# Optimization experiments

Measured on AMD Instinct MI355X. Metric: run time of the kernel, lower is better.

The kernel has to match this reference:

```python
import jax, jax.numpy as jnp
import numpy as np

B, S, H, E, K = 2, 2048, 1024, 8, 2
CAP_FACTOR = 1.5

def setup_inputs() -> dict:
    key = jax.random.key(0)
    ks = jax.random.split(key, 8)
    sd1 = 1.0 / np.sqrt(H)
    sd2 = 1.0 / np.sqrt(H + E)
    return {
        'hidden_states': jax.random.normal(ks[0], (B, S, H), dtype=jnp.float32),
        'w1': jax.random.normal(ks[1], (H, H), dtype=jnp.float32) * sd1,
        'b1': jnp.zeros((H,), jnp.float32),
        'w2': jax.random.normal(ks[2], (H, E), dtype=jnp.float32) * sd1,
        'b2': jnp.zeros((E,), jnp.float32),
        'wc1': jax.random.normal(ks[3], (H + E, H), dtype=jnp.float32) * sd2,
        'bc1': jnp.zeros((H,), jnp.float32),
        'wc2': jax.random.normal(ks[4], (H, E), dtype=jnp.float32) * sd1,
        'bc2': jnp.zeros((E,), jnp.float32),
        'cache_hit_rates': jax.random.uniform(ks[5], (E,), dtype=jnp.float32),
    }

def reference(hidden_states, w1, b1, w2, b2, wc1, bc1, wc2, bc2, cache_hit_rates):
    b, s, h = hidden_states.shape
    # router MLP: Linear -> ReLU -> Linear
    router_logits = jax.nn.relu(hidden_states @ w1 + b1) @ w2 + b2  # [B,S,E]
    # cache-aware adjustment
    avg_features = hidden_states.mean(axis=1)  # [B,H]
    combined = jnp.concatenate(
        [avg_features, jnp.broadcast_to(cache_hit_rates[None, :], (b, E))], axis=-1)
    adj = jnp.tanh(jax.nn.relu(combined @ wc1 + bc1) @ wc2 + bc2)  # [B,E]
    router_logits = router_logits + adj[:, None, :]
    router_probs = jax.nn.softmax(router_logits, axis=-1)  # [B,S,E]
    top_k_probs, top_k_indices = jax.lax.top_k(router_probs, K)  # [B,S,K]
    top_k_probs = top_k_probs / (top_k_probs.sum(axis=-1, keepdims=True) + 1e-8)
    capacity = int(b * s * CAP_FACTOR * K / E)
    # flatten in (b, s, k) order to replicate serial capacity counters
    N = b * s * K
    e_flat = top_k_indices.reshape(N)
    p_flat = top_k_probs.reshape(N)
    tok = jnp.arange(N) // K  # token index b*S+s
    onehot = jax.nn.one_hot(e_flat, E, dtype=jnp.int32)  # [N,E] small
    prior = jnp.cumsum(onehot, axis=0) - onehot  # exclusive count per expert
    pos = prior[jnp.arange(N), e_flat]  # slot within expert
    keep = pos < capacity
    posc = jnp.minimum(pos, capacity - 1)
    val = keep.astype(router_probs.dtype)
    dispatch = jnp.zeros((b * s, E, capacity), router_probs.dtype)
    dispatch = dispatch.at[tok, e_flat, posc].add(val).reshape(b, s, E, capacity)
    combine = jnp.zeros((b * s, E, capacity), router_probs.dtype)
    combine = combine.at[tok, e_flat, posc].add(val * p_flat).reshape(b, s, E, capacity)
    # load balancing aux loss
    router_prob_per_expert = router_probs.mean(axis=(0, 1))  # [E]
    expert_usage_rate = onehot.astype(router_probs.dtype).mean(axis=0)  # [E]
    aux_loss = jnp.sum(router_prob_per_expert * expert_usage_rate) * E
    return dispatch, combine, router_probs, aux_loss
```

## Files before the change

### kernel.cpp

```cpp
#include <hip/hip_runtime.h>
#include <hip/hip_bf16.h>

#define BB 2
#define SS 2048
#define HH 1024
#define EE 8
#define KK 2
#define CAP 1536
#define NTOK (BB * SS)
#define NASSIGN (NTOK * KK)

#define WS_PSUM   0
#define WS_AVG    8
#define WS_HC     2056
#define WS_ADJ    4104
#define WS_P1     4120
#define WS_P2     8216
#define WS_IDX    12312
#define WS_LOGITS 16408
#define WS_ZERO_FLOATS 4112
#define WS_ZERO_BYTES 16448
#define WS_BF16_BYTE 196704
#define WS_H_BYTE (WS_BF16_BYTE + 31457280)
#define WS_NEED (WS_H_BYTE + 16777216ull)

using short8 = __attribute__((ext_vector_type(8))) short;
using u16x8  = __attribute__((ext_vector_type(8))) unsigned short;
using f32x4  = __attribute__((ext_vector_type(4))) float;

__device__ __forceinline__ unsigned short f2bf(float f) {
  unsigned u = __float_as_uint(f);
  unsigned r = (u + 0x7fffu + ((u >> 16) & 1u)) >> 16;
  return (unsigned short)r;
}
__device__ __forceinline__ float bf2f(unsigned short h) {
  return __uint_as_float((unsigned)h << 16);
}
__device__ __forceinline__ void split3(float x, unsigned short& h,
                                       unsigned short& m, unsigned short& l) {
  h = f2bf(x);
  float r = x - bf2f(h);
  m = f2bf(r);
  l = f2bf(r - bf2f(m));
}

__device__ __forceinline__ void gload_lds16(const void* g, void* l) {
  __builtin_amdgcn_global_load_lds(
      (const __attribute__((address_space(1))) void*)g,
      (__attribute__((address_space(3))) void*)l, 16, 0, 0);
}

#define PREPX_BLKS 4096
#define PREPW_BLKS 256
#define AVG_BLKS   128
__global__ __launch_bounds__(256) void k_prep(
    const float* __restrict__ x, const float* __restrict__ w1,
    unsigned short* __restrict__ Xh, unsigned short* __restrict__ Xm,
    unsigned short* __restrict__ Xl,
    unsigned short* __restrict__ Wh, unsigned short* __restrict__ Wm,
    unsigned short* __restrict__ Wl,
    float* __restrict__ wshead, float* __restrict__ avg_part) {
  __shared__ unsigned short Th[64 * 65], Tm[64 * 65], Tl[64 * 65];
  int tid = threadIdx.x;
  int bid = blockIdx.x;
  if (bid < PREPX_BLKS) {
    if (bid == 0)
      for (int j = tid; j < WS_ZERO_FLOATS; j += 256) wshead[j] = 0.f;
    int i = (bid * 256 + tid) * 4;
    float4 v = *(const float4*)&x[i];
    unsigned short h[4], m[4], l[4];
    split3(v.x, h[0], m[0], l[0]);
    split3(v.y, h[1], m[1], l[1]);
    split3(v.z, h[2], m[2], l[2]);
    split3(v.w, h[3], m[3], l[3]);
    *(ushort4*)&Xh[i] = make_ushort4(h[0], h[1], h[2], h[3]);
    *(ushort4*)&Xm[i] = make_ushort4(m[0], m[1], m[2], m[3]);
    *(ushort4*)&Xl[i] = make_ushort4(l[0], l[1], l[2], l[3]);
  } else if (bid < PREPX_BLKS + PREPW_BLKS) {
    int pid = bid - PREPX_BLKS;
    int k0 = (pid & 15) * 64, n0 = (pid >> 4) * 64;
    for (int i = 0; i < 16; ++i) {
      int e = i * 256 + tid;
      int k = e >> 6, n = e & 63;
      float v = w1[(size_t)(k0 + k) * HH + n0 + n];
      unsigned short h, m, l;
      split3(v, h, m, l);
      Th[n * 65 + k] = h; Tm[n * 65 + k] = m; Tl[n * 65 + k] = l;
    }
    __syncthreads();
    for (int i = 0; i < 16; ++i) {
      int e = i * 256 + tid;
      int n = e >> 6, k = e & 63;
      size_t o = (size_t)(n0 + n) * HH + k0 + k;
      Wh[o] = Th[n * 65 + k]; Wm[o] = Tm[n * 65 + k]; Wl[o] = Tl[n * 65 + k];
    }
  } else {
    int pid = bid - PREPX_BLKS - PREPW_BLKS;
    int h = (pid & 3) * 256 + tid;
    int c = (pid >> 2) & 15;
    int b = pid >> 6;
    const float* p = x + (size_t)b * SS * HH + (size_t)(c * 128) * HH + h;
    float s = 0.f;
    for (int i = 0; i < 128; ++i) s += p[(size_t)i * HH];
    avg_part[(c * BB + b) * HH + h] = s;
  }
}

__global__ void k_avgp(const float* __restrict__ x, float* __restrict__ avg_part) {
  int h = blockIdx.x * 256 + threadIdx.x;
  int c = blockIdx.y;
  int b = blockIdx.z;
  const float* p = x + (size_t)b * SS * HH + (size_t)(c * 128) * HH + h;
  float s = 0.f;
  for (int i = 0; i < 128; ++i) s += p[(size_t)i * HH];
  avg_part[(c * BB + b) * HH + h] = s;
}

__global__ void k_hc(const float* __restrict__ avg_part, const float* __restrict__ chr,
                     const float* __restrict__ wc1, float* __restrict__ hc_raw) {
  __shared__ float avg_s[128];
  int tid = threadIdx.x;
  int j = blockIdx.x * 256 + tid;
  int c = blockIdx.y;
  int b = blockIdx.z;
  if (tid < 128) {
    float s = 0.f;
    for (int cc = 0; cc < 16; ++cc)
      s += avg_part[(cc * BB + b) * HH + c * 128 + tid];
    avg_s[tid] = s * (1.0f / SS);
  }
  __syncthreads();
  float acc = 0.f;
  for (int il = 0; il < 128; ++il)
    acc += avg_s[il] * wc1[(size_t)(c * 128 + il) * HH + j];
  if (c == 7)
    for (int i = 0; i < EE; ++i)
      acc += chr[i] * wc1[(size_t)(HH + i) * HH + j];
  atomicAdd(&hc_raw[b * HH + j], acc);
}

__global__ void k_adj(const float* __restrict__ hc_raw, const float* __restrict__ bc1,
                      const float* __restrict__ wc2, const float* __restrict__ bc2,
                      float* __restrict__ adj) {
  int b = blockIdx.x;
  int tid = threadIdx.x;
  float part[EE] = {};
  for (int j = tid; j < HH; j += 256) {
    float v = fmaxf(hc_raw[b * HH + j] + bc1[j], 0.f);
    for (int e = 0; e < EE; ++e) part[e] += v * wc2[j * EE + e];
  }
  for (int m = 1; m < 64; m <<= 1)
    for (int e = 0; e < EE; ++e) part[e] += __shfl_xor(part[e], m);
  __shared__ float red[4][EE];
  int wave = tid >> 6, lane = tid & 63;
  if (lane == 0)
    for (int e = 0; e < EE; ++e) red[wave][e] = part[e];
  __syncthreads();
  if (tid < EE) {
    float s = bc2[tid];
    for (int w = 0; w < 4; ++w) s += red[w][tid];
    adj[b * EE + tid] = tanhf(s);
  }
}

#define BM 128
#define BN 64
#define BK 32
#define ZF4_PER_BLOCK 49152
__global__ __launch_bounds__(256) void k_gemm_mfma(
    const unsigned short* __restrict__ Xh, const unsigned short* __restrict__ Xm,
    const unsigned short* __restrict__ Xl,
    const unsigned short* __restrict__ Wh, const unsigned short* __restrict__ Wm,
    const unsigned short* __restrict__ Wl,
    const float* __restrict__ b1, float* __restrict__ hbuf,
    f32x4* __restrict__ zout,
    const float* __restrict__ hc_raw, const float* __restrict__ bc1,
    const float* __restrict__ wc2, const float* __restrict__ bc2,
    float* __restrict__ adj) {
  __shared__ unsigned short As[3][BM * BK];
  __shared__ unsigned short Bs[3][BN * BK];
  __shared__ float b1s[BN];
  __shared__ float red[4][EE];
  int tid = threadIdx.x;

  if (blockIdx.y == HH / BN) {
    if (blockIdx.x >= BB) return;
    int b = blockIdx.x;
    float part[EE] = {};
    for (int j = tid; j < HH; j += 256) {
      float v = fmaxf(hc_raw[b * HH + j] + bc1[j], 0.f);
      for (int e = 0; e < EE; ++e) part[e] += v * wc2[j * EE + e];
    }
    for (int m = 1; m < 64; m <<= 1)
      for (int e = 0; e < EE; ++e) part[e] += __shfl_xor(part[e], m);
    int wave = tid >> 6, lane = tid & 63;
    if (lane == 0)
      for (int e = 0; e < EE; ++e) red[wave][e] = part[e];
    __syncthreads();
    if (tid < EE) {
      float s = bc2[tid];
      for (int w = 0; w < 4; ++w) s += red[w][tid];
      adj[b * EE + tid] = tanhf(s);
    }
    return;
  }

  int m0 = blockIdx.x * BM, n0 = blockIdx.y * BN;
  if (tid < BN) b1s[tid] = b1[n0 + tid];

  int bid = blockIdx.y * gridDim.x + blockIdx.x;
  f32x4* zp = zout + (size_t)bid * ZF4_PER_BLOCK;
  const f32x4 z4 = {0.f, 0.f, 0.f, 0.f};

  int lane = tid & 63, wave = tid >> 6;
  int wm = wave & 1, wn = wave >> 1;
  int q = lane >> 4, mr = lane & 15;
  int lr = lane >> 2, lq = lane & 3;

  f32x4 acc[4][2] = {};

  const unsigned short* Ag[3] = {Xh, Xm, Xl};
  const unsigned short* Bg[3] = {Wh, Wm, Wl};

  for (int k0 = 0; k0 < HH; k0 += BK) {
    __syncthreads();
#pragma unroll
    for (int j = 0; j < 6; ++j) {
      int i = wave + 4 * j;
      int s = i >> 3, g = i & 7;
      const unsigned short* gp =
          Ag[s] + (size_t)(m0 + g * 16 + lr) * HH + k0 + lq * 8;
      gload_lds16(gp, &As[s][g * 512]);
    }
#pragma unroll
    for (int j = 0; j < 3; ++j) {
      int i = wave + 4 * j;
      int s = i >> 2, g = i & 3;
      const unsigned short* gp =
          Bg[s] + (size_t)(n0 + g * 16 + lr) * HH + k0 + lq * 8;
      gload_lds16(gp, &Bs[s][g * 512]);
    }
    __syncthreads();

    {
      int ki = k0 >> 5;
      f32x4* zb = zp + ki * (256 * 6) + tid;
#pragma unroll
      for (int j = 0; j < 6; ++j) __builtin_nontemporal_store(z4, &zb[j * 256]);
    }

    short8 af[3][4], bf[3][2];
#pragma unroll
    for (int s = 0; s < 3; ++s) {
#pragma unroll
      for (int mi = 0; mi < 4; ++mi)
        af[s][mi] = *(const short8*)&As[s][(wm * 64 + mi * 16 + mr) * BK + q * 8];
#pragma unroll
      for (int ni = 0; ni < 2; ++ni)
        bf[s][ni] = *(const short8*)&Bs[s][(wn * 32 + ni * 16 + mr) * BK + q * 8];
    }
#pragma unroll
    for (int mi = 0; mi < 4; ++mi)
#pragma unroll
      for (int ni = 0; ni < 2; ++ni) {
        f32x4 c = acc[mi][ni];
        c = __builtin_amdgcn_mfma_f32_16x16x32_bf16(af[0][mi], bf[0][ni], c, 0, 0, 0);
        c = __builtin_amdgcn_mfma_f32_16x16x32_bf16(af[0][mi], bf[1][ni], c, 0, 0, 0);
        c = __builtin_amdgcn_mfma_f32_16x16x32_bf16(af[1][mi], bf[0][ni], c, 0, 0, 0);
        c = __builtin_amdgcn_mfma_f32_16x16x32_bf16(af[0][mi], bf[2][ni], c, 0, 0, 0);
        c = __builtin_amdgcn_mfma_f32_16x16x32_bf16(af[2][mi], bf[0][ni], c, 0, 0, 0);
        c = __builtin_amdgcn_mfma_f32_16x16x32_bf16(af[1][mi], bf[1][ni], c, 0, 0, 0);
        acc[mi][ni] = c;
      }
  }

#pragma unroll
  for (int ni = 0; ni < 2; ++ni) {
    int cloc = wn * 32 + ni * 16 + mr;
    int col = n0 + cloc;
    float bv = b1s[cloc];
#pragma unroll
    for (int mi = 0; mi < 4; ++mi)
#pragma unroll
      for (int r = 0; r < 4; ++r) {
        int row = m0 + wm * 64 + mi * 16 + q * 4 + r;
        hbuf[(size_t)row * HH + col] = fmaxf(acc[mi][ni][r] + bv, 0.f);
      }
  }
}

__global__ __launch_bounds__(256) void k_logits(
    const float* __restrict__ h, const float* __restrict__ w2,
    const float* __restrict__ b2, const float* __restrict__ adj,
    float* __restrict__ probs_out, int* __restrict__ idx_pack,
    float* __restrict__ p1o, float* __restrict__ p2o, float* __restrict__ psum) {
  __shared__ float w2s[HH * EE];
  __shared__ float ps[EE];
  int tid = threadIdx.x;
#pragma unroll
  for (int j = 0; j < 8; ++j)
    ((float4*)w2s)[tid + 256 * j] = ((const float4*)w2)[tid + 256 * j];
  if (tid < EE) ps[tid] = 0.f;
  __syncthreads();

  int lane = tid & 63, wave = tid >> 6;
  int t = blockIdx.x * 4 + wave;
  float acc[EE] = {};
  const float* hr = h + (size_t)t * HH;
#pragma unroll
  for (int i = 0; i < 16; ++i) {
    int e = lane + 64 * i;
    float hv = hr[e];
    float4 wa = ((const float4*)w2s)[2 * e];
    float4 wb = ((const float4*)w2s)[2 * e + 1];
    acc[0] += hv * wa.x; acc[1] += hv * wa.y; acc[2] += hv * wa.z; acc[3] += hv * wa.w;
    acc[4] += hv * wb.x; acc[5] += hv * wb.y; acc[6] += hv * wb.z; acc[7] += hv * wb.w;
  }
#pragma unroll
  for (int m = 1; m < 64; m <<= 1)
#pragma unroll
    for (int e = 0; e < EE; ++e) acc[e] += __shfl_xor(acc[e], m);

  if (lane == 0) {
    int b = t >> 11;
    float l[EE];
    float mx = -1e30f;
    for (int e = 0; e < EE; ++e) {
      l[e] = acc[e] + b2[e] + adj[b * EE + e];
      mx = fmaxf(mx, l[e]);
    }
    float s = 0.f;
    for (int e = 0; e < EE; ++e) { l[e] = expf(l[e] - mx); s += l[e]; }
    float inv = 1.f / s;
    for (int e = 0; e < EE; ++e) { l[e] *= inv; probs_out[t * EE + e] = l[e]; }
    int e1 = 0; float p1 = l[0];
    for (int e = 1; e < EE; ++e) if (l[e] > p1) { p1 = l[e]; e1 = e; }
    int e2 = -1; float p2 = -1.f;
    for (int e = 0; e < EE; ++e) if (e != e1 && l[e] > p2) { p2 = l[e]; e2 = e; }
    float norm = 1.f / (p1 + p2 + 1e-8f);
    idx_pack[t] = e1 | (e2 << 8);
    p1o[t] = p1 * norm;
    p2o[t] = p2 * norm;
    for (int e = 0; e < EE; ++e) atomicAdd(&ps[e], l[e]);
  }
  __syncthreads();
  if (tid < EE) atomicAdd(&psum[tid], ps[tid]);
}

__global__ __launch_bounds__(256) void k_gemm_f32(
    const float* __restrict__ X, const float* __restrict__ w1,
    const float* __restrict__ b1, const float* __restrict__ w2,
    float* __restrict__ logits) {
  __shared__ float Asf[16][65];
  __shared__ float Bsf[16][64];
  __shared__ float w2sf[64][EE];
  int tid = threadIdx.x;
  int m0 = blockIdx.x * 64, n0 = blockIdx.y * 64;
  for (int i = tid; i < 64 * EE; i += 256)
    w2sf[i / EE][i % EE] = w2[(size_t)(n0 + i / EE) * EE + (i % EE)];
  float acc[4][4] = {};
  int tx = tid & 15, ty = tid >> 4;
  for (int k0 = 0; k0 < HH; k0 += 16) {
    for (int idx = tid; idx < 64 * 16; idx += 256) {
      int m = idx >> 4, kk = idx & 15;
      Asf[kk][m] = X[(size_t)(m0 + m) * HH + k0 + kk];
    }
    for (int idx = tid; idx < 16 * 64; idx += 256) {
      int kk = idx >> 6, n = idx & 63;
      Bsf[kk][n] = w1[(size_t)(k0 + kk) * HH + n0 + n];
    }
    __syncthreads();
    for (int kk = 0; kk < 16; ++kk) {
      float a[4], bb[4];
      for (int i = 0; i < 4; ++i) a[i] = Asf[kk][ty * 4 + i];
      for (int j = 0; j < 4; ++j) bb[j] = Bsf[kk][tx * 4 + j];
      for (int i = 0; i < 4; ++i)
        for (int j = 0; j < 4; ++j) acc[i][j] += a[i] * bb[j];
    }
    __syncthreads();
  }
  float p[4][EE] = {};
  for (int i = 0; i < 4; ++i)
    for (int j = 0; j < 4; ++j) {
      int c = tx * 4 + j;
      float v = fmaxf(acc[i][j] + b1[n0 + c], 0.f);
      for (int e = 0; e < EE; ++e) p[i][e] += v * w2sf[c][e];
    }
  for (int m = 1; m < 16; m <<= 1)
    for (int i = 0; i < 4; ++i)
      for (int e = 0; e < EE; ++e) p[i][e] += __shfl_xor(p[i][e], m);
  if (tx == 0)
    for (int i = 0; i < 4; ++i)
      for (int e = 0; e < EE; ++e)
        atomicAdd(&logits[(size_t)(m0 + ty * 4 + i) * EE + e], p[i][e]);
}

__global__ void k_init_logits(const float* __restrict__ adj, const float* __restrict__ b2,
                              float* __restrict__ logits) {
  int i = blockIdx.x * 256 + threadIdx.x;
  int e = i & 7;
  int t = i >> 3;
  int b = t >> 11;
  logits[i] = b2[e] + adj[b * EE + e];
}

__global__ void k_softmax(const float* __restrict__ logits, float* __restrict__ probs_out,
                          int* __restrict__ idx_pack, float* __restrict__ p1o,
                          float* __restrict__ p2o, float* __restrict__ psum) {
  int t = blockIdx.x * 256 + threadIdx.x;
  float l[EE];
  float mx = -1e30f;
  for (int e = 0; e < EE; ++e) { l[e] = logits[t * EE + e]; mx = fmaxf(mx, l[e]); }
  float s = 0.f;
  for (int e = 0; e < EE; ++e) { l[e] = expf(l[e] - mx); s += l[e]; }
  float inv = 1.f / s;
  for (int e = 0; e < EE; ++e) { l[e] *= inv; probs_out[t * EE + e] = l[e]; }
  int e1 = 0; float p1 = l[0];
  for (int e = 1; e < EE; ++e) if (l[e] > p1) { p1 = l[e]; e1 = e; }
  int e2 = -1; float p2 = -1.f;
  for (int e = 0; e < EE; ++e) if (e != e1 && l[e] > p2) { p2 = l[e]; e2 = e; }
  float norm = 1.f / (p1 + p2 + 1e-8f);
  idx_pack[t] = e1 | (e2 << 8);
  p1o[t] = p1 * norm;
  p2o[t] = p2 * norm;
  for (int m = 1; m < 64; m <<= 1)
    for (int e = 0; e < EE; ++e) l[e] += __shfl_xor(l[e], m);
  if ((threadIdx.x & 63) == 0)
    for (int e = 0; e < EE; ++e) atomicAdd(&psum[e], l[e]);
}

__global__ __launch_bounds__(256) void k_route(
    const int* __restrict__ idx_pack, const float* __restrict__ p1,
    const float* __restrict__ p2, const float* __restrict__ psum,
    float* __restrict__ disp, float* __restrict__ comb, float* __restrict__ aux_out) {
  __shared__ int cnt[256][EE];
  __shared__ int tot[EE];
  int tid = threadIdx.x;
  const int CH = NASSIGN / 256;
  int n0 = tid * CH;
  int local[EE] = {};
  for (int n = n0; n < n0 + CH; ++n) {
    int t = n >> 1;
    int pk = idx_pack[t];
    int e = (n & 1) ? (pk >> 8) : (pk & 0xff);
    local[e]++;
  }
  for (int e = 0; e < EE; ++e) cnt[tid][e] = local[e];
  __syncthreads();
  if (tid < EE) {
    int run = 0;
    for (int t = 0; t < 256; ++t) { int v = cnt[t][tid]; cnt[t][tid] = run; run += v; }
    tot[tid] = run;
  }
  __syncthreads();
  int off[EE];
  for (int e = 0; e < EE; ++e) off[e] = cnt[tid][e];
  for (int n = n0; n < n0 + CH; ++n) {
    int t = n >> 1;
    int pk = idx_pack[t];
    int e; float p;
    if (n & 1) { e = pk >> 8; p = p2[t]; } else { e = pk & 0xff; p = p1[t]; }
    int pos = off[e]++;
    if (pos < CAP) {
      size_t o = (size_t)t * EE * CAP + (size_t)e * CAP + pos;
      disp[o] = 1.0f;
      comb[o] = p;
    }
  }
  if (tid == 0) {
    float aux = 0.f;
    for (int e = 0; e < EE; ++e)
      aux += (psum[e] / (float)NTOK) * ((float)tot[e] / (float)NASSIGN);
    aux_out[0] = aux * (float)EE;
  }
}

extern "C" void kernel_launch(void* const* d_in, const int* in_sizes, int n_in,
                              void* d_out, int out_size, void* d_ws, size_t ws_size,
                              hipStream_t stream) {
  const float* x   = (const float*)d_in[0];
  const float* w1  = (const float*)d_in[1];
  const float* b1  = (const float*)d_in[2];
  const float* w2  = (const float*)d_in[3];
  const float* b2  = (const float*)d_in[4];
  const float* wc1 = (const float*)d_in[5];
  const float* bc1 = (const float*)d_in[6];
  const float* wc2 = (const float*)d_in[7];
  const float* bc2 = (const float*)d_in[8];
  const float* chr = (const float*)d_in[9];

  float* out = (float*)d_out;
  float* disp  = out;
  float* comb  = disp + (size_t)NTOK * EE * CAP;
  float* probs = comb + (size_t)NTOK * EE * CAP;
  float* aux   = probs + (size_t)NTOK * EE;

  float* ws = (float*)d_ws;
  float* psum   = ws + WS_PSUM;
  float* hcr    = ws + WS_HC;
  float* adj    = ws + WS_ADJ;
  float* p1     = ws + WS_P1;
  float* p2     = ws + WS_P2;
  int*   idxp   = (int*)(ws + WS_IDX);
  float* logits = ws + WS_LOGITS;
  float* avgp   = ws + WS_LOGITS;

  char* wsb = (char*)d_ws;
  unsigned short* Xh = (unsigned short*)(wsb + WS_BF16_BYTE);
  unsigned short* Xm = Xh + (size_t)NTOK * HH;
  unsigned short* Xl = Xm + (size_t)NTOK * HH;
  unsigned short* Wh = Xl + (size_t)NTOK * HH;
  unsigned short* Wm = Wh + (size_t)HH * HH;
  unsigned short* Wl = Wm + (size_t)HH * HH;
  float* hbuf = (float*)(wsb + WS_H_BYTE);

  bool use_mfma = ws_size >= WS_NEED;

  if (use_mfma) {
    k_prep<<<PREPX_BLKS + PREPW_BLKS + AVG_BLKS, 256, 0, stream>>>(
        x, w1, Xh, Xm, Xl, Wh, Wm, Wl, ws, avgp);
    k_hc<<<dim3(HH / 256, 8, BB), 256, 0, stream>>>(avgp, chr, wc1, hcr);
    k_gemm_mfma<<<dim3(NTOK / BM, HH / BN + 1), 256, 0, stream>>>(
        Xh, Xm, Xl, Wh, Wm, Wl, b1, hbuf, (f32x4*)d_out,
        hcr, bc1, wc2, bc2, adj);
    k_logits<<<NTOK / 4, 256, 0, stream>>>(hbuf, w2, b2, adj, probs, idxp, p1, p2, psum);
  } else {
    hipMemsetAsync(d_ws, 0, WS_ZERO_BYTES, stream);
    hipMemsetAsync(d_out, 0, (size_t)out_size * sizeof(float), stream);
    k_avgp<<<dim3(HH / 256, 16, BB), 256, 0, stream>>>(x, avgp);
    k_hc<<<dim3(HH / 256, 8, BB), 256, 0, stream>>>(avgp, chr, wc1, hcr);
    k_adj<<<BB, 256, 0, stream>>>(hcr, bc1, wc2, bc2, adj);
    k_init_logits<<<(NTOK * EE) / 256, 256, 0, stream>>>(adj, b2, logits);
    k_gemm_f32<<<dim3(NTOK / 64, HH / 64), 256, 0, stream>>>(x, w1, b1, w2, logits);
    k_softmax<<<NTOK / 256, 256, 0, stream>>>(logits, probs, idxp, p1, p2, psum);
  }
  k_route<<<1, 256, 0, stream>>>(idxp, p1, p2, psum, disp, comb, aux);
}
```

Baseline: 509.3 us.

## Fuse cache-adjust MLP into GEMM grid and routing into logits via last-block counters

Removes the separate k_hc launch by computing the cache-adjust hidden layer in spare blocks of the MFMA GEMM grid. The last of those blocks, detected with an atomic counter, computes adj. The serial k_route launch is folded into k_logits: the last block to finish does the per-expert prefix count, capacity scatter and aux loss. This cuts kernel launches and gaps, but the counters must be zeroed before each call (presumably in k_prep), and the routing tail still runs on a single block.

```diff
diff --git a/kernel.cpp b/kernel.cpp
--- a/kernel.cpp
+++ b/kernel.cpp
@@ -11,7 +11,8 @@
 #define NASSIGN (NTOK * KK)
 
 #define WS_PSUM   0
-#define WS_AVG    8
+#define WS_CTR    8
+#define WS_AVG    16
 #define WS_HC     2056
 #define WS_ADJ    4104
 #define WS_P1     4120
@@ -106,63 +107,6 @@
   }
 }
 
-__global__ void k_avgp(const float* __restrict__ x, float* __restrict__ avg_part) {
-  int h = blockIdx.x * 256 + threadIdx.x;
-  int c = blockIdx.y;
-  int b = blockIdx.z;
-  const float* p = x + (size_t)b * SS * HH + (size_t)(c * 128) * HH + h;
-  float s = 0.f;
-  for (int i = 0; i < 128; ++i) s += p[(size_t)i * HH];
-  avg_part[(c * BB + b) * HH + h] = s;
-}
-
-__global__ void k_hc(const float* __restrict__ avg_part, const float* __restrict__ chr,
-                     const float* __restrict__ wc1, float* __restrict__ hc_raw) {
-  __shared__ float avg_s[128];
-  int tid = threadIdx.x;
-  int j = blockIdx.x * 256 + tid;
-  int c = blockIdx.y;
-  int b = blockIdx.z;
-  if (tid < 128) {
-    float s = 0.f;
-    for (int cc = 0; cc < 16; ++cc)
-      s += avg_part[(cc * BB + b) * HH + c * 128 + tid];
-    avg_s[tid] = s * (1.0f / SS);
-  }
-  __syncthreads();
-  float acc = 0.f;
-  for (int il = 0; il < 128; ++il)
-    acc += avg_s[il] * wc1[(size_t)(c * 128 + il) * HH + j];
-  if (c == 7)
-    for (int i = 0; i < EE; ++i)
-      acc += chr[i] * wc1[(size_t)(HH + i) * HH + j];
-  atomicAdd(&hc_raw[b * HH + j], acc);
-}
-
-__global__ void k_adj(const float* __restrict__ hc_raw, const float* __restrict__ bc1,
-                      const float* __restrict__ wc2, const float* __restrict__ bc2,
-                      float* __restrict__ adj) {
-  int b = blockIdx.x;
-  int tid = threadIdx.x;
-  float part[EE] = {};
-  for (int j = tid; j < HH; j += 256) {
-    float v = fmaxf(hc_raw[b * HH + j] + bc1[j], 0.f);
-    for (int e = 0; e < EE; ++e) part[e] += v * wc2[j * EE + e];
-  }
-  for (int m = 1; m < 64; m <<= 1)
-    for (int e = 0; e < EE; ++e) part[e] += __shfl_xor(part[e], m);
-  __shared__ float red[4][EE];
-  int wave = tid >> 6, lane = tid & 63;
-  if (lane == 0)
-    for (int e = 0; e < EE; ++e) red[wave][e] = part[e];
-  __syncthreads();
-  if (tid < EE) {
-    float s = bc2[tid];
-    for (int w = 0; w < 4; ++w) s += red[w][tid];
-    adj[b * EE + tid] = tanhf(s);
-  }
-}
-
 #define BM 128
 #define BN 64
 #define BK 32
@@ -174,22 +118,53 @@
     const unsigned short* __restrict__ Wl,
     const float* __restrict__ b1, float* __restrict__ hbuf,
     f32x4* __restrict__ zout,
-    const float* __restrict__ hc_raw, const float* __restrict__ bc1,
+    const float* __restrict__ avg_part, const float* __restrict__ chr,
+    const float* __restrict__ wc1, const float* __restrict__ bc1,
     const float* __restrict__ wc2, const float* __restrict__ bc2,
-    float* __restrict__ adj) {
+    float* __restrict__ hc_raw, float* __restrict__ adj,
+    int* __restrict__ ctr) {
   __shared__ unsigned short As[3][BM * BK];
   __shared__ unsigned short Bs[3][BN * BK];
   __shared__ float b1s[BN];
   __shared__ float red[4][EE];
+  __shared__ int sflag;
   int tid = threadIdx.x;
 
   if (blockIdx.y == HH / BN) {
-    if (blockIdx.x >= BB) return;
-    int b = blockIdx.x;
+    int b  = blockIdx.x & 1;
+    int j0 = (blockIdx.x >> 1) * 64;
+    float* avgs  = (float*)&As[0][0];
+    float* hcred = (float*)&Bs[0][0];
+    for (int k = 0; k < 4; ++k) {
+      int i = tid * 4 + k;
+      float s = 0.f;
+#pragma unroll
+      for (int cc = 0; cc < 16; ++cc) s += avg_part[(cc * BB + b) * HH + i];
+      avgs[i] = s * (1.0f / SS);
+    }
+    __syncthreads();
+    int p = tid >> 6, jj = tid & 63, j = j0 + jj;
+    float acc = 0.f;
+    for (int i = p * 258; i < p * 258 + 258; ++i) {
+      float a = (i < HH) ? avgs[i] : chr[i - HH];
+      acc += a * wc1[(size_t)i * HH + j];
+    }
+    hcred[p * 64 + jj] = acc;
+    __syncthreads();
+    if (tid < 64) {
+      float s = hcred[tid] + hcred[64 + tid] + hcred[128 + tid] + hcred[192 + tid];
+      hc_raw[b * HH + j0 + tid] = s;
+    }
+    __threadfence();
+    __syncthreads();
+    if (tid == 0) sflag = (atomicAdd(&ctr[b], 1) == 15);
+    __syncthreads();
+    if (!sflag) return;
+    __threadfence();
     float part[EE] = {};
-    for (int j = tid; j < HH; j += 256) {
-      float v = fmaxf(hc_raw[b * HH + j] + bc1[j], 0.f);
-      for (int e = 0; e < EE; ++e) part[e] += v * wc2[j * EE + e];
+    for (int j2 = tid; j2 < HH; j2 += 256) {
+      float v = fmaxf(hc_raw[b * HH + j2] + bc1[j2], 0.f);
+      for (int e = 0; e < EE; ++e) part[e] += v * wc2[j2 * EE + e];
     }
     for (int m = 1; m < 64; m <<= 1)
       for (int e = 0; e < EE; ++e) part[e] += __shfl_xor(part[e], m);
@@ -293,9 +268,13 @@
     const float* __restrict__ h, const float* __restrict__ w2,
     const float* __restrict__ b2, const float* __restrict__ adj,
     float* __restrict__ probs_out, int* __restrict__ idx_pack,
-    float* __restrict__ p1o, float* __restrict__ p2o, float* __restrict__ psum) {
+    float* __restrict__ p1o, float* __restrict__ p2o, float* __restrict__ psum,
+    int* __restrict__ ctr,
+    float* __restrict__ disp, float* __restrict__ comb, float* __restrict__ aux_out) {
   __shared__ float w2s[HH * EE];
   __shared__ float ps[EE];
+  __shared__ int tot[EE];
+  __shared__ int sflag;
   int tid = threadIdx.x;
 #pragma unroll
   for (int j = 0; j < 8; ++j)
@@ -345,6 +324,109 @@
   }
   __syncthreads();
   if (tid < EE) atomicAdd(&psum[tid], ps[tid]);
+
+  __threadfence();
+  __syncthreads();
+  if (tid == 0) sflag = (atomicAdd(ctr, 1) == (int)gridDim.x - 1);
+  __syncthreads();
+  if (!sflag) return;
+  __threadfence();
+
+  int* cnt = (int*)w2s;
+  const int CH = NASSIGN / 256;
+  int n0 = tid * CH;
+  int local[EE] = {};
+  for (int n = n0; n < n0 + CH; ++n) {
+    int tt = n >> 1;
+    int pk = idx_pack[tt];
+    int e = (n & 1) ? (pk >> 8) : (pk & 0xff);
+    local[e]++;
+  }
+  for (int e = 0; e < EE; ++e) cnt[tid * EE + e] = local[e];
+  __syncthreads();
+  if (tid < EE) {
+    int run = 0;
+    for (int tt = 0; tt < 256; ++tt) { int v = cnt[tt * EE + tid]; cnt[tt * EE + tid] = run; run += v; }
+    tot[tid] = run;
+  }
+  __syncthreads();
+  int off[EE];
+  for (int e = 0; e < EE; ++e) off[e] = cnt[tid * EE + e];
+  for (int n = n0; n < n0 + CH; ++n) {
+    int tt = n >> 1;
+    int pk = idx_pack[tt];
+    int e; float p;
+    if (n & 1) { e = pk >> 8; p = p2o[tt]; } else { e = pk & 0xff; p = p1o[tt]; }
+    int pos = off[e]++;
+    if (pos < CAP) {
+      size_t o = (size_t)tt * EE * CAP + (size_t)e * CAP + pos;
+      disp[o] = 1.0f;
+      comb[o] = p;
+    }
+  }
+  if (tid == 0) {
+    float aux = 0.f;
+    for (int e = 0; e < EE; ++e)
+      aux += (psum[e] / (float)NTOK) * ((float)tot[e] / (float)NASSIGN);
+    aux_out[0] = aux * (float)EE;
+  }
+}
+
+__global__ void k_avgp(const float* __restrict__ x, float* __restrict__ avg_part) {
+  int h = blockIdx.x * 256 + threadIdx.x;
+  int c = blockIdx.y;
+  int b = blockIdx.z;
+  const float* p = x + (size_t)b * SS * HH + (size_t)(c * 128) * HH + h;
+  float s = 0.f;
+  for (int i = 0; i < 128; ++i) s += p[(size_t)i * HH];
+  avg_part[(c * BB + b) * HH + h] = s;
+}
+
+__global__ void k_hc(const float* __restrict__ avg_part, const float* __restrict__ chr,
+                     const float* __restrict__ wc1, float* __restrict__ hc_raw) {
+  __shared__ float avg_s[128];
+  int tid = threadIdx.x;
+  int j = blockIdx.x * 256 + tid;
+  int c = blockIdx.y;
+  int b = blockIdx.z;
+  if (tid < 128) {
+    float s = 0.f;
+    for (int cc = 0; cc < 16; ++cc)
+      s += avg_part[(cc * BB + b) * HH + c * 128 + tid];
+    avg_s[tid] = s * (1.0f / SS);
+  }
+  __syncthreads();
+  float acc = 0.f;
+  for (int il = 0; il < 128; ++il)
+    acc += avg_s[il] * wc1[(size_t)(c * 128 + il) * HH + j];
+  if (c == 7)
+    for (int i = 0; i < EE; ++i)
+      acc += chr[i] * wc1[(size_t)(HH + i) * HH + j];
+  atomicAdd(&hc_raw[b * HH + j], acc);
+}
+
+__global__ void k_adj(const float* __restrict__ hc_raw, const float* __restrict__ bc1,
+                      const float* __restrict__ wc2, const float* __restrict__ bc2,
+                      float* __restrict__ adj) {
+  int b = blockIdx.x;
+  int tid = threadIdx.x;
+  float part[EE] = {};
+  for (int j = tid; j < HH; j += 256) {
+    float v = fmaxf(hc_raw[b * HH + j] + bc1[j], 0.f);
+    for (int e = 0; e < EE; ++e) part[e] += v * wc2[j * EE + e];
+  }
+  for (int m = 1; m < 64; m <<= 1)
+    for (int e = 0; e < EE; ++e) part[e] += __shfl_xor(part[e], m);
+  __shared__ float red[4][EE];
+  int wave = tid >> 6, lane = tid & 63;
+  if (lane == 0)
+    for (int e = 0; e < EE; ++e) red[wave][e] = part[e];
+  __syncthreads();
+  if (tid < EE) {
+    float s = bc2[tid];
+    for (int w = 0; w < 4; ++w) s += red[w][tid];
+    adj[b * EE + tid] = tanhf(s);
+  }
 }
 
 __global__ __launch_bounds__(256) void k_gemm_f32(
@@ -497,6 +579,7 @@
 
   float* ws = (float*)d_ws;
   float* psum   = ws + WS_PSUM;
+  int*   ctr    = (int*)(ws + WS_CTR);
   float* hcr    = ws + WS_HC;
   float* adj    = ws + WS_ADJ;
   float* p1     = ws + WS_P1;
@@ -519,11 +602,11 @@
   if (use_mfma) {
     k_prep<<<PREPX_BLKS + PREPW_BLKS + AVG_BLKS, 256, 0, stream>>>(
         x, w1, Xh, Xm, Xl, Wh, Wm, Wl, ws, avgp);
-    k_hc<<<dim3(HH / 256, 8, BB), 256, 0, stream>>>(avgp, chr, wc1, hcr);
     k_gemm_mfma<<<dim3(NTOK / BM, HH / BN + 1), 256, 0, stream>>>(
         Xh, Xm, Xl, Wh, Wm, Wl, b1, hbuf, (f32x4*)d_out,
-        hcr, bc1, wc2, bc2, adj);
-    k_logits<<<NTOK / 4, 256, 0, stream>>>(hbuf, w2, b2, adj, probs, idxp, p1, p2, psum);
+        avgp, chr, wc1, bc1, wc2, bc2, hcr, adj, ctr);
+    k_logits<<<NTOK / 4, 256, 0, stream>>>(hbuf, w2, b2, adj, probs, idxp, p1, p2,
+                                           psum, ctr + 2, disp, comb, aux);
   } else {
     hipMemsetAsync(d_ws, 0, WS_ZERO_BYTES, stream);
     hipMemsetAsync(d_out, 0, (size_t)out_size * sizeof(float), stream);
@@ -533,6 +616,6 @@
     k_init_logits<<<(NTOK * EE) / 256, 256, 0, stream>>>(adj, b2, logits);
     k_gemm_f32<<<dim3(NTOK / 64, HH / 64), 256, 0, stream>>>(x, w1, b1, w2, logits);
     k_softmax<<<NTOK / 256, 256, 0, stream>>>(logits, probs, idxp, p1, p2, psum);
-  }
-  k_route<<<1, 256, 0, stream>>>(idxp, p1, p2, psum, disp, comb, aux);
-}
+    k_route<<<1, 256, 0, stream>>>(idxp, p1, p2, psum, disp, comb, aux);
+  }
+}
```

New measurement: 606.6 us. +19.1%, slower.
